# Kernel optimization log

Measured on AMD Instinct MI355X. Metric: run time of the kernel, lower is better.

## Reference

```python
import jax, jax.numpy as jnp
import numpy as np

DT = 0.04  # CFG.dt in the original repo (Euler step for FitzHugh-Nagumo)


def _fhn_scan(z, dt):
    """Integrate FitzHugh-Nagumo dynamics over time.
    z: (B, T, N) input current per timestep. Returns V: (B, T, N), with V[:,0]=0.
    V[k] = (1+dt)V[k-1] - dt/3 V[k-1]^3 - dt S[k-1] + dt z[k-1]
    S[k] = S[k-1] + dt*0.08*(V[k-1] + 0.7 - 0.8 S[k-1])
    """
    B, T, N = z.shape
    z_t = jnp.transpose(z, (1, 0, 2))  # (T, B, N), time-major for scan

    def step(carry, z_prev):
        V, S = carry
        Vn = (1.0 + dt) * V - (dt / 3.0) * (V ** 3) - dt * S + dt * z_prev
        Sn = S + dt * 0.08 * (V + 0.7 - 0.8 * S)
        return (Vn, Sn), Vn

    init = (jnp.zeros((B, N), z.dtype), jnp.zeros((B, N), z.dtype))
    _, Vs = jax.lax.scan(step, init, z_t[:-1])  # (T-1, B, N): V[1:]
    V = jnp.concatenate([jnp.zeros((1, B, N), z.dtype), Vs], axis=0)
    return jnp.transpose(V, (1, 0, 2))  # (B, T, N)


def setup_inputs() -> dict:
    key = jax.random.key(0)
    k1, k2, k3 = jax.random.split(key, 3)
    B, T = 64, 2048
    batch = jax.random.normal(k1, (B, T, 784), dtype=jnp.float32)
    # nn.Linear default init: U(-1/sqrt(fan_in), 1/sqrt(fan_in))
    W1 = jax.random.uniform(k2, (100, 784), jnp.float32, -1.0, 1.0) / np.sqrt(784.0)
    W2 = jax.random.uniform(k3, (10, 100), jnp.float32, -1.0, 1.0) / np.sqrt(100.0)
    return {"batch": batch, "W1": W1, "W2": W2}


def reference(batch, W1, W2):
    dt = DT
    z1 = jnp.einsum('btd,nd->btn', batch, W1)  # (B, T, 100)
    V1 = _fhn_scan(z1, dt)                      # (B, T, 100)
    z2 = jnp.einsum('btn,mn->btm', V1 * 0.5, W2)  # (B, T, 10)
    V2 = _fhn_scan(z2, dt)                      # (B, T, 10)
    return V2
```

## Files before the change

kernel.cpp:

```cpp
#include <hip/hip_runtime.h>
#include <hip/hip_bf16.h>


#define FHN_DT 0.04f

typedef _Float16 f16x8 __attribute__((ext_vector_type(8)));
typedef __attribute__((ext_vector_type(4))) float f32x4;

__device__ __forceinline__ void gl16(const void* g, void* l) {
    __builtin_amdgcn_global_load_lds(
        (const __attribute__((address_space(1))) unsigned int*)g,
        (__attribute__((address_space(3))) unsigned int*)l, 16, 0, 0);
}

__device__ __forceinline__ void sync_lds() {
    asm volatile("s_waitcnt lgkmcnt(0)" ::: "memory");
    __builtin_amdgcn_s_barrier();
    asm volatile("" ::: "memory");
}

__global__ void prep_w16(const float* __restrict__ W1, unsigned short* __restrict__ Wg) {
    int idx = blockIdx.x * 256 + threadIdx.x;
    if (idx >= 179200) return;
    int kt   = idx / 7168;
    int rem  = idx % 7168;
    int f    = rem >> 9;
    int r2   = rem & 511;
    int l    = r2 >> 3;
    int e    = r2 & 7;
    int term = f / 7, ct = f % 7;
    int n = ct * 16 + (l & 15);
    int k = kt * 32 + (l >> 4) * 8 + e;
    float v = (n < 100 && k < 784) ? W1[n * 784 + k] : 0.0f;
    _Float16 h = (_Float16)v;
    unsigned short o;
    if (term == 0) o = __builtin_bit_cast(unsigned short, h);
    else           o = __builtin_bit_cast(unsigned short, (_Float16)((v - (float)h) * 1024.0f));
    Wg[idx] = o;
}

__global__ __launch_bounds__(512, 1) void gemm1_w(const float* __restrict__ A,
                                                  const unsigned short* __restrict__ Wg,
                                                  float* __restrict__ z1p) {
    __shared__ __align__(16) char smem[129024];
    const int tid  = threadIdx.x;
    const int w    = tid >> 6;
    const int lane = tid & 63;
    const int ln   = lane & 15;
    const int kg   = lane >> 4;
    const long row0 = (long)blockIdx.x * 256;

    const float* arow0 = A + (row0 + w * 32 + ln) * 784 + kg * 8;
    const float* arow1 = arow0 + (size_t)16 * 784;

    f32x4 acc1[2][7] = {};
    f32x4 acc2[2][7] = {};
    float afpA[16], afpB[16];

#define ISSUE_A(T, AF) {                                                        \
        if ((T) == 24 && kg >= 2) {                                             \
            *(float4*)&AF[0]  = make_float4(0.f, 0.f, 0.f, 0.f);                \
            *(float4*)&AF[4]  = make_float4(0.f, 0.f, 0.f, 0.f);                \
            *(float4*)&AF[8]  = make_float4(0.f, 0.f, 0.f, 0.f);                \
            *(float4*)&AF[12] = make_float4(0.f, 0.f, 0.f, 0.f);                \
        } else {                                                                \
            *(float4*)&AF[0]  = *(const float4*)(arow0 + (T) * 32);             \
            *(float4*)&AF[4]  = *(const float4*)(arow0 + (T) * 32 + 4);         \
            *(float4*)&AF[8]  = *(const float4*)(arow1 + (T) * 32);             \
            *(float4*)&AF[12] = *(const float4*)(arow1 + (T) * 32 + 4);         \
        } }

#define LOADSEC(TS, NB) {                                                       \
        const char* src_ = (const char*)Wg + (size_t)(TS) * 14336;              \
        _Pragma("unroll 1")                                                     \
        for (int c_ = 0; c_ < (NB) / 8192; ++c_)                                \
            gl16(src_ + c_ * 8192 + tid * 16, smem + c_ * 8192 + tid * 16);     \
        if (((NB) & 8191) != 0 && tid * 16 < ((NB) & 8191))                     \
            gl16(src_ + ((NB) / 8192) * 8192 + tid * 16,                        \
                 smem + ((NB) / 8192) * 8192 + tid * 16);                       \
    }

#define SEC_SYNC() {                                                            \
        asm volatile("s_waitcnt vmcnt(0)" ::: "memory");                        \
        __builtin_amdgcn_s_barrier();                                           \
        asm volatile("" ::: "memory");                                          \
    }

#define BODY(KT, AF, TS) {                                                      \
        f16x8 ah0, al0, ah1, al1;                                               \
        _Pragma("unroll")                                                       \
        for (int e_ = 0; e_ < 8; ++e_) {                                        \
            float a0_ = AF[e_], a1_ = AF[8 + e_];                               \
            _Float16 h0_ = (_Float16)a0_, h1_ = (_Float16)a1_;                  \
            ah0[e_] = h0_; ah1[e_] = h1_;                                       \
            al0[e_] = (_Float16)((a0_ - (float)h0_) * 1024.0f);                 \
            al1[e_] = (_Float16)((a1_ - (float)h1_) * 1024.0f);                 \
        }                                                                       \
        if ((KT) < 23) ISSUE_A((KT) + 2, AF);                                   \
        const char* cb_ = smem + ((KT) - (TS)) * 14336 + lane * 16;             \
        _Pragma("unroll")                                                       \
        for (int ct_ = 0; ct_ < 7; ++ct_) {                                     \
            f16x8 bh = *(const f16x8*)(cb_ + ct_ * 1024);                       \
            f16x8 bl = *(const f16x8*)(cb_ + 7168 + ct_ * 1024);                \
            acc1[0][ct_] = __builtin_amdgcn_mfma_f32_16x16x32_f16(ah0, bh, acc1[0][ct_], 0, 0, 0); \
            acc2[0][ct_] = __builtin_amdgcn_mfma_f32_16x16x32_f16(ah0, bl, acc2[0][ct_], 0, 0, 0); \
            acc2[0][ct_] = __builtin_amdgcn_mfma_f32_16x16x32_f16(al0, bh, acc2[0][ct_], 0, 0, 0); \
            acc1[1][ct_] = __builtin_amdgcn_mfma_f32_16x16x32_f16(ah1, bh, acc1[1][ct_], 0, 0, 0); \
            acc2[1][ct_] = __builtin_amdgcn_mfma_f32_16x16x32_f16(ah1, bl, acc2[1][ct_], 0, 0, 0); \
            acc2[1][ct_] = __builtin_amdgcn_mfma_f32_16x16x32_f16(al1, bh, acc2[1][ct_], 0, 0, 0); \
        } }

    ISSUE_A(0, afpA);
    ISSUE_A(1, afpB);

    LOADSEC(0, 129024);
    SEC_SYNC();
#pragma unroll 1
    for (int k0 = 0; k0 < 8; k0 += 2) { BODY(k0, afpA, 0); BODY(k0 + 1, afpB, 0); }
    BODY(8, afpA, 0);

    asm volatile("" ::: "memory");
    __builtin_amdgcn_s_barrier();
    asm volatile("" ::: "memory");
    LOADSEC(9, 114688);
    SEC_SYNC();
#pragma unroll 1
    for (int k0 = 9; k0 < 17; k0 += 2) { BODY(k0, afpB, 9); BODY(k0 + 1, afpA, 9); }

    asm volatile("" ::: "memory");
    __builtin_amdgcn_s_barrier();
    asm volatile("" ::: "memory");
    LOADSEC(17, 114688);
    SEC_SYNC();
#pragma unroll 1
    for (int k0 = 17; k0 < 25; k0 += 2) { BODY(k0, afpB, 17); BODY(k0 + 1, afpA, 17); }

#pragma unroll
    for (int ct = 0; ct < 7; ++ct) {
        int n = ct * 16 + ln;
        if (n < 100) {
#pragma unroll
            for (int rt = 0; rt < 2; ++rt) {
                long rg = row0 + w * 32 + rt * 16 + kg * 4;
                float* p = z1p + rg * 100 + n;
#pragma unroll
                for (int r = 0; r < 4; ++r)
                    p[r * 100] = fmaf(acc2[rt][ct][r], 0.0009765625f, acc1[rt][ct][r]);
            }
        }
    }
#undef ISSUE_A
#undef LOADSEC
#undef SEC_SYNC
#undef BODY
}

__global__ __launch_bounds__(576) void fused_scan3(const float* __restrict__ z1p,
                                                   const float* __restrict__ W2,
                                                   float* __restrict__ out) {
    __shared__ float fsm[32768];
    const int tid = threadIdx.x;
    const int b   = blockIdx.x;
    const float dt = FHN_DT;

    float V = 0.f, S = 0.f;
    const float* zb = z1p + (long)b * 2048 * 100 + tid;
    float z0[16], z1r[16], z2r[16], z3r[16];
    if (tid < 100) {
#pragma unroll
        for (int u = 0; u < 16; ++u) {
            z0[u]  = zb[u * 100];
            z1r[u] = zb[(16 + u) * 100];
            z2r[u] = zb[(32 + u) * 100];
            z3r[u] = zb[(48 + u) * 100];
        }
    }

    const int tg = tid - 128;
    int pp = (tg >> 7) & 3;
    pp = __builtin_amdgcn_readfirstlane(pp);
    const int r  = tg & 127;
    const int mb = (pp == 0) ? 0 : (pp == 1 ? 4 : 7);
    const int mc = (pp == 0) ? 4 : 3;
    const int m2 = tid - 512;

    for (int i = 0; i <= 18; ++i) {
        if (tid < 128) {
            bool a1 = (tid < 100) && (i < 16);
            if (a1) {
#pragma unroll
                for (int sub = 0; sub < 8; ++sub) {
                    float zt[16];
                    int tn = (i * 8 + sub + 4) * 16;
                    if (tn < 2048) {
#pragma unroll
                        for (int u = 0; u < 16; ++u) zt[u] = zb[(tn + u) * 100];
                    }
                    const int cw = i & 1;
#pragma unroll
                    for (int u = 0; u < 16; ++u) {
                        int tl = sub * 16 + u;
                        fsm[cw * 14848 + tl * 116 + tid] = V;
                        float z  = z0[u];
                        float V3 = V * V * V;
                        float Vn = fmaf(1.f + dt, V,
                                    fmaf(-dt / 3.f, V3, fmaf(-dt, S, dt * z)));
                        float Sn = fmaf(dt * 0.08f, V + 0.7f - 0.8f * S, S);
                        V = Vn; S = Sn;
                    }
#pragma unroll
                    for (int u = 0; u < 16; ++u) {
                        z0[u] = z1r[u]; z1r[u] = z2r[u]; z2r[u] = z3r[u]; z3r[u] = zt[u];
                    }
                }
            }
        } else if (tid < 512) {
            if (i >= 1 && i <= 16) {
                const int pb = (i - 1) & 1;
                float acc[4] = {0.f, 0.f, 0.f, 0.f};
                for (int kq = 0; kq < 25; ++kq) {
                    float4 v = *(const float4*)&fsm[pb * 14848 + r * 116 + kq * 4];
#pragma unroll
                    for (int j = 0; j < 4; ++j) {
                        if (j < mc) {
                            const float* wp = W2 + (mb + j) * 100 + kq * 4;
                            acc[j] = fmaf(v.x, wp[0], acc[j]);
                            acc[j] = fmaf(v.y, wp[1], acc[j]);
                            acc[j] = fmaf(v.z, wp[2], acc[j]);
                            acc[j] = fmaf(v.w, wp[3], acc[j]);
                        }
                    }
                }
#pragma unroll
                for (int j = 0; j < 4; ++j)
                    if (j < mc) fsm[29696 + pb * 1536 + r * 12 + mb + j] = 0.5f * acc[j];
            }
            if (i >= 3) {
                const int pb = (i - 1) & 1;
                float* dst = out + ((long)b * 2048 + (long)(i - 3) * 128 + r) * 10;
#pragma unroll
                for (int j = 0; j < 4; ++j)
                    if (j < mc) dst[mb + j] = fsm[pb * 14848 + r * 116 + 100 + mb + j];
            }
        } else {
            bool a2 = (m2 < 10) && (i >= 2) && (i < 18);
            if (a2) {
                const int cw = i & 1;
#pragma unroll
                for (int sub = 0; sub < 8; ++sub) {
                    float z0s[16];
#pragma unroll
                    for (int u = 0; u < 16; ++u)
                        z0s[u] = fsm[29696 + cw * 1536 + (sub * 16 + u) * 12 + m2];
#pragma unroll
                    for (int u = 0; u < 16; ++u) {
                        int tl = sub * 16 + u;
                        fsm[cw * 14848 + tl * 116 + 100 + m2] = V;
                        float z  = z0s[u];
                        float V3 = V * V * V;
                        float Vn = fmaf(1.f + dt, V,
                                    fmaf(-dt / 3.f, V3, fmaf(-dt, S, dt * z)));
                        float Sn = fmaf(dt * 0.08f, V + 0.7f - 0.8f * S, S);
                        V = Vn; S = Sn;
                    }
                }
            }
        }
        sync_lds();
    }
}

extern "C" void kernel_launch(void* const* d_in, const int* in_sizes, int n_in,
                              void* d_out, int out_size, void* d_ws, size_t ws_size,
                              hipStream_t stream) {
    const float* batch = (const float*)d_in[0];
    const float* W1    = (const float*)d_in[1];
    const float* W2    = (const float*)d_in[2];
    float* out = (float*)d_out;

    char* base = (char*)d_ws;
    unsigned short* Wg = (unsigned short*)base;
    float* z1p = (float*)(base + 358400);

    prep_w16<<<700, 256, 0, stream>>>(W1, Wg);
    gemm1_w<<<512, 512, 0, stream>>>(batch, Wg, z1p);
    fused_scan3<<<64, 576, 0, stream>>>(z1p, W2, out);
}
```

Before: 188.7 us.

## Halve GEMM1 rows per block and stage W1 in five smaller LDS sections

Each block of the first GEMM now covers 128 rows instead of 256, with one 16-row tile per wave instead of two, and the grid doubles to 1024 blocks. Weights are staged through LDS in five equal sections of five k-tiles (70 KB) instead of three larger ones (126 KB). The launch bound now requests 4 blocks per CU. The aim is to cut register and LDS use so more blocks can overlap their weight-staging barriers with other blocks' compute, instead of one block per CU stalling. The cost is that every block reloads the full weight matrix, doubling weight traffic, and less data is reused per LDS load.

Measured after the change: 205.3 us. 1.09x slower.

```diff
diff --git a/kernel.cpp b/kernel.cpp
--- a/kernel.cpp
+++ b/kernel.cpp
@@ -39,45 +39,39 @@
     Wg[idx] = o;
 }
 
-__global__ __launch_bounds__(512, 1) void gemm1_w(const float* __restrict__ A,
+__global__ __launch_bounds__(512, 4) void gemm1_x(const float* __restrict__ A,
                                                   const unsigned short* __restrict__ Wg,
                                                   float* __restrict__ z1p) {
-    __shared__ __align__(16) char smem[129024];
+    __shared__ __align__(16) char smem[71680];
     const int tid  = threadIdx.x;
     const int w    = tid >> 6;
     const int lane = tid & 63;
     const int ln   = lane & 15;
     const int kg   = lane >> 4;
-    const long row0 = (long)blockIdx.x * 256;
-
-    const float* arow0 = A + (row0 + w * 32 + ln) * 784 + kg * 8;
-    const float* arow1 = arow0 + (size_t)16 * 784;
-
-    f32x4 acc1[2][7] = {};
-    f32x4 acc2[2][7] = {};
-    float afpA[16], afpB[16];
+    const long row0 = (long)blockIdx.x * 128;
+
+    const float* arow = A + (row0 + w * 16 + ln) * 784 + kg * 8;
+
+    f32x4 acc1[7] = {};
+    f32x4 acc2[7] = {};
+    float afpA[8], afpB[8];
 
 #define ISSUE_A(T, AF) {                                                        \
         if ((T) == 24 && kg >= 2) {                                             \
-            *(float4*)&AF[0]  = make_float4(0.f, 0.f, 0.f, 0.f);                \
-            *(float4*)&AF[4]  = make_float4(0.f, 0.f, 0.f, 0.f);                \
-            *(float4*)&AF[8]  = make_float4(0.f, 0.f, 0.f, 0.f);                \
-            *(float4*)&AF[12] = make_float4(0.f, 0.f, 0.f, 0.f);                \
+            *(float4*)&AF[0] = make_float4(0.f, 0.f, 0.f, 0.f);                 \
+            *(float4*)&AF[4] = make_float4(0.f, 0.f, 0.f, 0.f);                 \
         } else {                                                                \
-            *(float4*)&AF[0]  = *(const float4*)(arow0 + (T) * 32);             \
-            *(float4*)&AF[4]  = *(const float4*)(arow0 + (T) * 32 + 4);         \
-            *(float4*)&AF[8]  = *(const float4*)(arow1 + (T) * 32);             \
-            *(float4*)&AF[12] = *(const float4*)(arow1 + (T) * 32 + 4);         \
+            *(float4*)&AF[0] = *(const float4*)(arow + (T) * 32);               \
+            *(float4*)&AF[4] = *(const float4*)(arow + (T) * 32 + 4);           \
         } }
 
-#define LOADSEC(TS, NB) {                                                       \
+#define LOADSEC(TS) {                                                           \
         const char* src_ = (const char*)Wg + (size_t)(TS) * 14336;              \
         _Pragma("unroll 1")                                                     \
-        for (int c_ = 0; c_ < (NB) / 8192; ++c_)                                \
+        for (int c_ = 0; c_ < 8; ++c_)                                          \
             gl16(src_ + c_ * 8192 + tid * 16, smem + c_ * 8192 + tid * 16);     \
-        if (((NB) & 8191) != 0 && tid * 16 < ((NB) & 8191))                     \
-            gl16(src_ + ((NB) / 8192) * 8192 + tid * 16,                        \
-                 smem + ((NB) / 8192) * 8192 + tid * 16);                       \
+        if (tid < 384)                                                          \
+            gl16(src_ + 65536 + tid * 16, smem + 65536 + tid * 16);             \
     }
 
 #define SEC_SYNC() {                                                            \
@@ -87,14 +81,13 @@
     }
 
 #define BODY(KT, AF, TS) {                                                      \
-        f16x8 ah0, al0, ah1, al1;                                               \
+        f16x8 ah, al;                                                           \
         _Pragma("unroll")                                                       \
         for (int e_ = 0; e_ < 8; ++e_) {                                        \
-            float a0_ = AF[e_], a1_ = AF[8 + e_];                               \
-            _Float16 h0_ = (_Float16)a0_, h1_ = (_Float16)a1_;                  \
-            ah0[e_] = h0_; ah1[e_] = h1_;                                       \
-            al0[e_] = (_Float16)((a0_ - (float)h0_) * 1024.0f);                 \
-            al1[e_] = (_Float16)((a1_ - (float)h1_) * 1024.0f);                 \
+            float a_ = AF[e_];                                                  \
+            _Float16 h_ = (_Float16)a_;                                         \
+            ah[e_] = h_;                                                        \
+            al[e_] = (_Float16)((a_ - (float)h_) * 1024.0f);                    \
         }                                                                       \
         if ((KT) < 23) ISSUE_A((KT) + 2, AF);                                   \
         const char* cb_ = smem + ((KT) - (TS)) * 14336 + lane * 16;             \
@@ -102,57 +95,50 @@
         for (int ct_ = 0; ct_ < 7; ++ct_) {                                     \
             f16x8 bh = *(const f16x8*)(cb_ + ct_ * 1024);                       \
             f16x8 bl = *(const f16x8*)(cb_ + 7168 + ct_ * 1024);                \
-            acc1[0][ct_] = __builtin_amdgcn_mfma_f32_16x16x32_f16(ah0, bh, acc1[0][ct_], 0, 0, 0); \
-            acc2[0][ct_] = __builtin_amdgcn_mfma_f32_16x16x32_f16(ah0, bl, acc2[0][ct_], 0, 0, 0); \
-            acc2[0][ct_] = __builtin_amdgcn_mfma_f32_16x16x32_f16(al0, bh, acc2[0][ct_], 0, 0, 0); \
-            acc1[1][ct_] = __builtin_amdgcn_mfma_f32_16x16x32_f16(ah1, bh, acc1[1][ct_], 0, 0, 0); \
-            acc2[1][ct_] = __builtin_amdgcn_mfma_f32_16x16x32_f16(ah1, bl, acc2[1][ct_], 0, 0, 0); \
-            acc2[1][ct_] = __builtin_amdgcn_mfma_f32_16x16x32_f16(al1, bh, acc2[1][ct_], 0, 0, 0); \
+            acc1[ct_] = __builtin_amdgcn_mfma_f32_16x16x32_f16(ah, bh, acc1[ct_], 0, 0, 0); \
+            acc2[ct_] = __builtin_amdgcn_mfma_f32_16x16x32_f16(ah, bl, acc2[ct_], 0, 0, 0); \
+            acc2[ct_] = __builtin_amdgcn_mfma_f32_16x16x32_f16(al, bh, acc2[ct_], 0, 0, 0); \
         } }
+
+#define SECTION(TS, F0, F1) {                                                   \
+        if ((TS) > 0) {                                                         \
+            asm volatile("" ::: "memory");                                      \
+            __builtin_amdgcn_s_barrier();      \
+            asm volatile("" ::: "memory");                                      \
+        }                                                                       \
+        LOADSEC(TS);                                                            \
+        SEC_SYNC();                                                             \
+        BODY((TS) + 0, F0, TS);                                                 \
+        BODY((TS) + 1, F1, TS);                                                 \
+        BODY((TS) + 2, F0, TS);                                                 \
+        BODY((TS) + 3, F1, TS);                                                 \
+        BODY((TS) + 4, F0, TS);                                                 \
+    }
 
     ISSUE_A(0, afpA);
     ISSUE_A(1, afpB);
 
-    LOADSEC(0, 129024);
-    SEC_SYNC();
-#pragma unroll 1
-    for (int k0 = 0; k0 < 8; k0 += 2) { BODY(k0, afpA, 0); BODY(k0 + 1, afpB, 0); }
-    BODY(8, afpA, 0);
-
-    asm volatile("" ::: "memory");
-    __builtin_amdgcn_s_barrier();
-    asm volatile("" ::: "memory");
-    LOADSEC(9, 114688);
-    SEC_SYNC();
-#pragma unroll 1
-    for (int k0 = 9; k0 < 17; k0 += 2) { BODY(k0, afpB, 9); BODY(k0 + 1, afpA, 9); }
-
-    asm volatile("" ::: "memory");
-    __builtin_amdgcn_s_barrier();
-    asm volatile("" ::: "memory");
-    LOADSEC(17, 114688);
-    SEC_SYNC();
-#pragma unroll 1
-    for (int k0 = 17; k0 < 25; k0 += 2) { BODY(k0, afpB, 17); BODY(k0 + 1, afpA, 17); }
+    SECTION(0,  afpA, afpB);
+    SECTION(5,  afpB, afpA);
+    SECTION(10, afpA, afpB);
+    SECTION(15, afpB, afpA);
+    SECTION(20, afpA, afpB);
 
 #pragma unroll
     for (int ct = 0; ct < 7; ++ct) {
         int n = ct * 16 + ln;
         if (n < 100) {
-#pragma unroll
-            for (int rt = 0; rt < 2; ++rt) {
-                long rg = row0 + w * 32 + rt * 16 + kg * 4;
-                float* p = z1p + rg * 100 + n;
-#pragma unroll
-                for (int r = 0; r < 4; ++r)
-                    p[r * 100] = fmaf(acc2[rt][ct][r], 0.0009765625f, acc1[rt][ct][r]);
-            }
+            float* p = z1p + (row0 + w * 16 + kg * 4) * 100 + n;
+#pragma unroll
+            for (int r = 0; r < 4; ++r)
+                p[r * 100] = fmaf(acc2[ct][r], 0.0009765625f, acc1[ct][r]);
         }
     }
 #undef ISSUE_A
 #undef LOADSEC
 #undef SEC_SYNC
 #undef BODY
+#undef SECTION
 }
 
 __global__ __launch_bounds__(576) void fused_scan3(const float* __restrict__ z1p,
@@ -283,6 +269,6 @@
     float* z1p = (float*)(base + 358400);
 
     prep_w16<<<700, 256, 0, stream>>>(W1, Wg);
-    gemm1_w<<<512, 512, 0, stream>>>(batch, Wg, z1p);
+    gemm1_x<<<1024, 512, 0, stream>>>(batch, Wg, z1p);
     fused_scan3<<<64, 576, 0, stream>>>(z1p, W2, out);
 }
```
